# Kernel optimization log

Measured on AMD Instinct MI355X. Metric: run time of the kernel, lower is better.

The kernel has to match this reference:

```python
import jax, jax.numpy as jnp
import numpy as np

N = 65536        # number of encoding vectors (flattened tokens)
K = 1024         # num_embeddings (codebook size)
D = 128          # embedding_dim
BETA = 0.25


def setup_inputs() -> dict:
    key = jax.random.key(0)
    k_enc, k_cb = jax.random.split(key)
    encoding = jax.random.normal(k_enc, (N, D), dtype=jnp.float32)
    # nn.Embedding weight initialized uniform(-1/K, 1/K)
    codebook = jax.random.uniform(k_cb, (K, D), dtype=jnp.float32,
                                  minval=-1.0 / K, maxval=1.0 / K)
    return {"encoding": encoding, "codebook": codebook}


def reference(encoding, codebook):
    # Nearest codebook entry per row. argmin of L2 distance == argmin of
    # squared distance; expand ||e - w||^2 = ||e||^2 - 2 e.w + ||w||^2.
    # ||e||^2 is constant per row, so it does not affect the argmin.
    scores = (-2.0 * jnp.einsum('nd,kd->nk', encoding, codebook)
              + jnp.sum(codebook * codebook, axis=-1)[None, :])  # [N, K]
    quantized_index = jnp.argmin(scores, axis=-1)                # [N] int
    quantized_embedding = codebook[quantized_index]              # [N, D] gather == onehot @ W

    sg = jax.lax.stop_gradient
    commitment_loss = jnp.mean((sg(quantized_embedding) - encoding) ** 2)
    embedding_loss = jnp.mean((quantized_embedding - sg(encoding)) ** 2)
    vq_loss = commitment_loss * BETA + embedding_loss

    # straight-through estimator
    quantized_st = encoding + sg(quantized_embedding - encoding)

    quantized_index = quantized_index[:, None]  # match torch unsqueeze(1) -> [N, 1]
    return (quantized_index, quantized_st, vq_loss, embedding_loss, commitment_loss)
```

## Files before the change

kernel.cpp:

```cpp
#include <hip/hip_runtime.h>


#define NROWS 65536
#define KCB   1024
#define DIM   128
#define DV    32
#define MSE_DENOM 8388608.0f
#define MARGIN 3.0e-5f
#define MARGINS 0.030720f
#define FLAGCAP 16384
#define CSCALE   1024.0f
#define CDESCALE 0.0009765625f

#define WS_CNORM_F  256
#define WS_CN1024_F 1280
#define WS_LIST_B   12288
#define WS_PH_B     77824
#define WS_NEEDED   339968

typedef __attribute__((ext_vector_type(16))) float float16v;
typedef _Float16 half8 __attribute__((ext_vector_type(8)));
union U4H8 { uint4 u; half8 h; };
union F4A  { float4 v; float f[4]; };
union F16V { float16v v; float f[16]; };
union HU   { _Float16 f; unsigned short u; };

__device__ __forceinline__ float fmed3(float a, float b, float c) {
  return __builtin_amdgcn_fmed3f(a, b, c);
}
__device__ __forceinline__ void gload16(const void* g, void* s) {
  __builtin_amdgcn_global_load_lds((const __attribute__((address_space(1))) unsigned int*)g,
                                   (__attribute__((address_space(3))) unsigned int*)s,
                                   16, 0, 0);
}

__global__ __launch_bounds__(64) void vq_prep0(const float* __restrict__ C,
                                               float* __restrict__ wsf) {
  int k = blockIdx.x * 64 + threadIdx.x;
  if (k == 0) { wsf[0] = 0.0f; ((unsigned*)wsf)[1] = 0u; }
  const float4* c4 = (const float4*)C + (size_t)k * DV;
  float s = 0.f;
#pragma unroll 8
  for (int i = 0; i < DV; ++i) {
    float4 v = c4[i];
    s = fmaf(v.x, v.x, s); s = fmaf(v.y, v.y, s);
    s = fmaf(v.z, v.z, s); s = fmaf(v.w, v.w, s);
  }
  wsf[WS_CNORM_F + k]  = s;
  wsf[WS_CN1024_F + k] = s * CSCALE;
}

__global__ __launch_bounds__(256) void vq_pack(const float* __restrict__ C,
                                               uint4* __restrict__ PH) {
  int g = blockIdx.x * 256 + threadIdx.x;
  int mt = g >> 9, s = (g >> 6) & 7, l = g & 63;
  int cw = mt * 32 + (l & 31);
  int k0 = s * 16 + (l >> 5) * 8;
  const float* src = C + (size_t)cw * DIM + k0;
  float4 x0 = *(const float4*)src;
  float4 x1 = *(const float4*)(src + 4);
  unsigned h[8];
  {
    float v[8] = {x0.x, x0.y, x0.z, x0.w, x1.x, x1.y, x1.z, x1.w};
#pragma unroll
    for (int j = 0; j < 8; ++j) { HU u; u.f = (_Float16)(CSCALE * v[j]); h[j] = u.u; }
  }
  PH[g] = make_uint4(h[0] | (h[1] << 16), h[2] | (h[3] << 16),
                     h[4] | (h[5] << 16), h[6] | (h[7] << 16));
}

__global__ __launch_bounds__(256, 4) void vq_main8(const float* __restrict__ E,
                                                   const float* __restrict__ C,
                                                   float* __restrict__ wsf,
                                                   float* __restrict__ out) {
  __shared__ uint4 SH[2][1024];
  __shared__ __align__(16) float CN[1024];
  __shared__ float X1[64], X2[64];
  __shared__ int   XI[64];
  __shared__ int   BI[64];

  const int tid  = threadIdx.x;
  const int w    = tid >> 6;
  const int l    = tid & 63;
  const int half = l >> 5;
  const int rr   = l & 31;
  const int pair = w >> 1;
  const int rw   = w & 1;
  const int row0 = blockIdx.x * 64;
  const int row  = row0 + rw * 32 + rr;

  const uint4* PHg = (const uint4*)((const char*)wsf + WS_PH_B);

  {
    uint4* base = &SH[0][0];
    gload16(PHg + tid,                  base + tid);
    gload16(PHg + 256 + tid,            base + 256 + tid);
    gload16(PHg + 16 * 512 + tid,       base + 512 + tid);
    gload16(PHg + 16 * 512 + 256 + tid, base + 768 + tid);
    gload16(((const uint4*)(wsf + WS_CN1024_F)) + tid, ((uint4*)CN) + tid);
  }

  half8 beh[8];
  float s2 = 0.f;
  const float* erow = E + (size_t)row * DIM + half * 8;
#pragma unroll
  for (int s = 0; s < 8; ++s) {
    float4 x0 = *(const float4*)(erow + s * 16);
    float4 x1 = *(const float4*)(erow + s * 16 + 4);
    float v[8] = {x0.x, x0.y, x0.z, x0.w, x1.x, x1.y, x1.z, x1.w};
#pragma unroll
    for (int j = 0; j < 8; ++j) {
      float y = v[j];
      s2 = fmaf(y, y, s2);
      beh[s][j] = (_Float16)(-2.f * y);
    }
  }

  asm volatile("s_waitcnt vmcnt(0)" ::: "memory");
  __syncthreads();

  float m1 = 3.0e38f, m2 = 3.0e38f;
  int   bi = 0;

  for (int st = 0; st < 16; ++st) {
    const int buf = st & 1;
    const int tg  = pair * 16 + st;
    if (st < 15) {
      uint4* nb = &SH[buf ^ 1][0];
      const uint4* s0 = PHg + (size_t)(st + 1) * 512;
      const uint4* s1 = PHg + (size_t)(17 + st) * 512;
      gload16(s0 + tid,       nb + tid);
      gload16(s0 + 256 + tid, nb + 256 + tid);
      gload16(s1 + tid,       nb + 512 + tid);
      gload16(s1 + 256 + tid, nb + 768 + tid);
    }

    F16V accA, accB;
#pragma unroll
    for (int q = 0; q < 4; ++q) {
      F4A c; c.v = *(const float4*)&CN[tg * 32 + q * 8 + half * 4];
      accA.f[q * 4 + 0] = c.f[0]; accA.f[q * 4 + 1] = c.f[1];
      accA.f[q * 4 + 2] = c.f[2]; accA.f[q * 4 + 3] = c.f[3];
    }
    accB.v = (float16v){0,0,0,0,0,0,0,0,0,0,0,0,0,0,0,0};
#pragma unroll
    for (int s = 0; s < 8; s += 2) {
      U4H8 h0, h1;
      h0.u = SH[buf][pair * 512 + s * 64 + l];
      h1.u = SH[buf][pair * 512 + (s + 1) * 64 + l];
      accA.v = __builtin_amdgcn_mfma_f32_32x32x16_f16(h0.h, beh[s],     accA.v, 0, 0, 0);
      accB.v = __builtin_amdgcn_mfma_f32_32x32x16_f16(h1.h, beh[s + 1], accB.v, 0, 0, 0);
    }

    const int kb = tg * 32 + half * 4;
#pragma unroll
    for (int reg = 0; reg < 16; ++reg) {
      float sc = accA.f[reg] + accB.f[reg];
      bool nb_ = sc < m1;
      m2 = fmed3(sc, m1, m2);
      m1 = fminf(sc, m1);
      bi = nb_ ? (kb + (reg >> 2) * 8 + (reg & 3)) : bi;
    }

    asm volatile("s_waitcnt vmcnt(0)" ::: "memory");
    __syncthreads();
  }

  {
    float om1 = __shfl_xor(m1, 32, 64);
    float om2 = __shfl_xor(m2, 32, 64);
    int   obi = __shfl_xor(bi, 32, 64);
    float nsv = fminf(fminf(m2, om2), fmaxf(m1, om1));
    if (om1 < m1 || (om1 == m1 && obi < bi)) { m1 = om1; bi = obi; }
    m2 = nsv;
  }
  float en = s2 + __shfl_xor(s2, 32, 64);

  if (pair == 1 && half == 0) {
    X1[rw * 32 + rr] = m1; X2[rw * 32 + rr] = m2; XI[rw * 32 + rr] = bi;
  }
  __syncthreads();

  if (pair == 0 && half == 0) {
    const int r = rw * 32 + rr;
    float xb = X1[r], xs = X2[r];
    int   xi = XI[r];
    float sv = fminf(fminf(m2, xs), fmaxf(m1, xb));
    if (xb < m1 || (xb == m1 && xi < bi)) { m1 = xb; bi = xi; }
    out[row] = (float)bi;
    BI[r] = bi;
    if (sv - m1 < MARGINS) {
      unsigned idx = atomicAdd((unsigned*)wsf + 1, 1u);
      if (idx < FLAGCAP) ((int*)((char*)wsf + WS_LIST_B))[idx] = row;
    }
    float term = fmaf(m1, CDESCALE, en);
#pragma unroll
    for (int off = 16; off > 0; off >>= 1) term += __shfl_down(term, off);
    if (rr == 0) atomicAdd(wsf, term);
  }
  __syncthreads();

  const float4* C4   = (const float4*)C;
  float4*       out4 = (float4*)out;
#pragma unroll
  for (int it = 0; it < 8; ++it) {
    int flat = it * 256 + tid;
    int r = flat >> 5, d4 = flat & 31;
    out4[(NROWS / 4) + (size_t)(row0 + r) * DV + d4] = C4[(size_t)BI[r] * DV + d4];
  }
}

__global__ __launch_bounds__(256) void vq_fix(const float* __restrict__ E,
                                              const float* __restrict__ C,
                                              float* __restrict__ wsf,
                                              float* __restrict__ out) {
  __shared__ float4 eL[4][32];
  __shared__ float  RV[4][4];
  __shared__ int    RI[4][4];
  __shared__ int    RESi[4];
  const int tid = threadIdx.x;
  const int wv  = tid >> 6;
  const int ln  = tid & 63;
  const int* list = (const int*)((const char*)wsf + WS_LIST_B);
  int nf = (int)((const unsigned*)wsf)[1];
  if (nf > FLAGCAP) nf = FLAGCAP;
  const float4* E4 = (const float4*)E;
  const float4* C4 = (const float4*)C;
  const float*  cn = wsf + WS_CNORM_F;
  float4* out4 = (float4*)out;

  for (int g = blockIdx.x; g * 4 < nf; g += gridDim.x) {
    const int base = g * 4;
    if (tid < 128) {
      int r = tid >> 5, d4 = tid & 31;
      int R = (base + r < nf) ? list[base + r] : list[base];
      eL[r][d4] = E4[(size_t)R * DV + d4];
    }
    __syncthreads();
    float bv[4] = {3.0e38f, 3.0e38f, 3.0e38f, 3.0e38f};
    int   bi[4] = {0, 0, 0, 0};
#pragma unroll
    for (int j = 0; j < 4; ++j) {
      int k = j * 256 + tid;
      float d0 = 0.f, d1 = 0.f, d2 = 0.f, d3 = 0.f;
#pragma unroll 4
      for (int d4 = 0; d4 < 32; ++d4) {
        float4 c = C4[(size_t)k * DV + d4];
        float4 e0 = eL[0][d4], e1 = eL[1][d4], e2 = eL[2][d4], e3 = eL[3][d4];
        d0 = fmaf(c.x, e0.x, d0); d0 = fmaf(c.y, e0.y, d0);
        d0 = fmaf(c.z, e0.z, d0); d0 = fmaf(c.w, e0.w, d0);
        d1 = fmaf(c.x, e1.x, d1); d1 = fmaf(c.y, e1.y, d1);
        d1 = fmaf(c.z, e1.z, d1); d1 = fmaf(c.w, e1.w, d1);
        d2 = fmaf(c.x, e2.x, d2); d2 = fmaf(c.y, e2.y, d2);
        d2 = fmaf(c.z, e2.z, d2); d2 = fmaf(c.w, e2.w, d2);
        d3 = fmaf(c.x, e3.x, d3); d3 = fmaf(c.y, e3.y, d3);
        d3 = fmaf(c.z, e3.z, d3); d3 = fmaf(c.w, e3.w, d3);
      }
      float cnk = cn[k];
      float s0 = fmaf(-2.f, d0, cnk);
      float s1 = fmaf(-2.f, d1, cnk);
      float s2 = fmaf(-2.f, d2, cnk);
      float s3 = fmaf(-2.f, d3, cnk);
      if (s0 < bv[0] || (s0 == bv[0] && k < bi[0])) { bv[0] = s0; bi[0] = k; }
      if (s1 < bv[1] || (s1 == bv[1] && k < bi[1])) { bv[1] = s1; bi[1] = k; }
      if (s2 < bv[2] || (s2 == bv[2] && k < bi[2])) { bv[2] = s2; bi[2] = k; }
      if (s3 < bv[3] || (s3 == bv[3] && k < bi[3])) { bv[3] = s3; bi[3] = k; }
    }
#pragma unroll
    for (int off = 32; off > 0; off >>= 1) {
#pragma unroll
      for (int r = 0; r < 4; ++r) {
        float wv_ = __shfl_down(bv[r], off);
        int   ji  = __shfl_down(bi[r], off);
        if (wv_ < bv[r] || (wv_ == bv[r] && ji < bi[r])) { bv[r] = wv_; bi[r] = ji; }
      }
    }
    if (ln == 0) {
#pragma unroll
      for (int r = 0; r < 4; ++r) { RV[wv][r] = bv[r]; RI[wv][r] = bi[r]; }
    }
    __syncthreads();
    if (tid < 4) {
      float v = RV[0][tid]; int i = RI[0][tid];
#pragma unroll
      for (int q = 1; q < 4; ++q) {
        float vv = RV[q][tid]; int ii = RI[q][tid];
        if (vv < v || (vv == v && ii < i)) { v = vv; i = ii; }
      }
      RESi[tid] = i;
      if (base + tid < nf) out[list[base + tid]] = (float)i;
    }
    __syncthreads();
    if (tid < 128) {
      int r = tid >> 5, d4 = tid & 31;
      if (base + r < nf) {
        int R = list[base + r];
        out4[(NROWS / 4) + (size_t)R * DV + d4] = C4[(size_t)RESi[r] * DV + d4];
      }
    }
    __syncthreads();
  }
}

__global__ void vq_final(const float* __restrict__ wsf, float* __restrict__ out) {
  if (threadIdx.x == 0 && blockIdx.x == 0) {
    float mse = wsf[0] / MSE_DENOM;
    out[NROWS + NROWS * DIM + 0] = 1.25f * mse;
    out[NROWS + NROWS * DIM + 1] = mse;
    out[NROWS + NROWS * DIM + 2] = mse;
  }
}

__global__ __launch_bounds__(256) void vq_prep_fb(const float* __restrict__ C,
                                                  float* __restrict__ ws) {
  int k = blockIdx.x * 256 + threadIdx.x;
  if (k == 0) ws[0] = 0.0f;
  const float4* c4 = (const float4*)C + (size_t)k * DV;
  float s = 0.f;
#pragma unroll 8
  for (int i = 0; i < DV; ++i) {
    float4 v = c4[i];
    s = fmaf(v.x, v.x, s); s = fmaf(v.y, v.y, s);
    s = fmaf(v.z, v.z, s); s = fmaf(v.w, v.w, s);
  }
  ws[64 + k] = s;
}

__global__ __launch_bounds__(256) void vq_main_fb(const float* __restrict__ E,
                                                  const float* __restrict__ C,
                                                  const float* __restrict__ cnorm,
                                                  float* __restrict__ out,
                                                  float* __restrict__ lossacc) {
  __shared__ float smem[16384];
  float4* EsV = (float4*)smem;
  float4* CsV = (float4*)(smem + 8192);
  const int tid  = threadIdx.x;
  const int row0 = blockIdx.x * 64;
#pragma unroll
  for (int i = 0; i < 8; ++i) {
    int flat = i * 256 + tid;
    int r = flat >> 5, d4 = flat & 31;
    EsV[r * 32 + (d4 ^ (r & 31))] = ((const float4*)E)[(size_t)(row0 + r) * DV + d4];
  }
  const int tx = tid & 15, ty = tid >> 4;
  int rbase[4], rmask[4];
#pragma unroll
  for (int i = 0; i < 4; ++i) { int r = i * 16 + ty; rbase[i] = r * 32; rmask[i] = r & 31; }
  float bestv[4]; int besti[4];
#pragma unroll
  for (int i = 0; i < 4; ++i) { bestv[i] = 3.0e38f; besti[i] = 0; }
  for (int ch = 0; ch < 16; ++ch) {
    const int k0 = ch * 64;
    __syncthreads();
#pragma unroll
    for (int i = 0; i < 8; ++i) {
      int flat = i * 256 + tid;
      int k = flat >> 5, d4 = flat & 31;
      CsV[k * 32 + (d4 ^ (k & 31))] = ((const float4*)C)[(size_t)(k0 + k) * DV + d4];
    }
    __syncthreads();
    float acc[4][4] = {};
#pragma unroll 8
    for (int d4 = 0; d4 < DV; ++d4) {
      float4 a[4], b[4];
#pragma unroll
      for (int i = 0; i < 4; ++i) a[i] = EsV[rbase[i] + (d4 ^ rmask[i])];
#pragma unroll
      for (int j = 0; j < 4; ++j) { int k = j * 16 + tx; b[j] = CsV[k * 32 + (d4 ^ (k & 31))]; }
#pragma unroll
      for (int i = 0; i < 4; ++i)
#pragma unroll
        for (int j = 0; j < 4; ++j) {
          acc[i][j] = fmaf(a[i].x, b[j].x, acc[i][j]);
          acc[i][j] = fmaf(a[i].y, b[j].y, acc[i][j]);
          acc[i][j] = fmaf(a[i].z, b[j].z, acc[i][j]);
          acc[i][j] = fmaf(a[i].w, b[j].w, acc[i][j]);
        }
    }
#pragma unroll
    for (int j = 0; j < 4; ++j) {
      int kg = k0 + j * 16 + tx;
      float cnv = cnorm[kg];
#pragma unroll
      for (int i = 0; i < 4; ++i) {
        float s = fmaf(-2.0f, acc[i][j], cnv);
        if (s < bestv[i] || (s == bestv[i] && kg < besti[i])) { bestv[i] = s; besti[i] = kg; }
      }
    }
  }
  float* Rv = smem + 8192;
  int*   Ri = (int*)(smem + 9216);
  int*   BIf = (int*)(smem + 10240);
  __syncthreads();
#pragma unroll
  for (int i = 0; i < 4; ++i) {
    int r = i * 16 + ty;
    Rv[r * 16 + tx] = bestv[i];
    Ri[r * 16 + tx] = besti[i];
  }
  __syncthreads();
  if (tid < 64) {
    const int r = tid;
    float bv = Rv[r * 16]; int bi = Ri[r * 16];
#pragma unroll
    for (int t = 1; t < 16; ++t) {
      float v = Rv[r * 16 + t]; int ii = Ri[r * 16 + t];
      if (v < bv || (v == bv && ii < bi)) { bv = v; bi = ii; }
    }
    float en = 0.f;
#pragma unroll 8
    for (int d4 = 0; d4 < DV; ++d4) {
      float4 v = EsV[r * 32 + (d4 ^ (r & 31))];
      en = fmaf(v.x, v.x, en); en = fmaf(v.y, v.y, en);
      en = fmaf(v.z, v.z, en); en = fmaf(v.w, v.w, en);
    }
    out[row0 + r] = (float)bi;
    BIf[r] = bi;
    float blocksum = en + bv;
#pragma unroll
    for (int off = 32; off > 0; off >>= 1) blocksum += __shfl_down(blocksum, off);
    if (tid == 0) atomicAdd(lossacc, blocksum);
  }
  __syncthreads();
  const float4* C4   = (const float4*)C;
  float4*       out4 = (float4*)out;
  for (int flat = tid; flat < 64 * DV; flat += 256) {
    int r = flat >> 5, d4 = flat & 31;
    out4[(NROWS / 4) + (size_t)(row0 + r) * DV + d4] = C4[(size_t)BIf[r] * DV + d4];
  }
}

__global__ void vq_final_fb(const float* __restrict__ ws, float* __restrict__ out) {
  if (threadIdx.x == 0 && blockIdx.x == 0) {
    float mse = ws[0] / MSE_DENOM;
    out[NROWS + NROWS * DIM + 0] = 1.25f * mse;
    out[NROWS + NROWS * DIM + 1] = mse;
    out[NROWS + NROWS * DIM + 2] = mse;
  }
}

extern "C" void kernel_launch(void* const* d_in, const int* in_sizes, int n_in,
                              void* d_out, int out_size, void* d_ws, size_t ws_size,
                              hipStream_t stream) {
  const float* E = (const float*)d_in[0];
  const float* C = (const float*)d_in[1];
  float* out = (float*)d_out;
  float* wsf = (float*)d_ws;

  if (ws_size >= (size_t)WS_NEEDED) {
    uint4* PH = (uint4*)((char*)d_ws + WS_PH_B);
    vq_prep0<<<16, 64, 0, stream>>>(C, wsf);
    vq_pack<<<64, 256, 0, stream>>>(C, PH);
    vq_main8<<<NROWS / 64, 256, 0, stream>>>(E, C, wsf, out);
    vq_fix<<<512, 256, 0, stream>>>(E, C, wsf, out);
    vq_final<<<1, 64, 0, stream>>>(wsf, out);
  } else {
    vq_prep_fb<<<4, 256, 0, stream>>>(C, wsf);
    vq_main_fb<<<NROWS / 64, 256, 0, stream>>>(E, C, wsf + 64, out, wsf);
    vq_final_fb<<<1, 64, 0, stream>>>(wsf, out);
  }
}
```

Measured before the change: 161.0 us.

## Triple-buffer codebook tiles in LDS and merge helper kernels to cut launches

The main kernel moves from double to triple buffering of the packed fp16 codebook tiles in LDS. It prefetches two stages ahead and waits with a partial vmcnt plus a single barrier per iteration, instead of a full drain and sync at the end of each step. The two prep kernels are merged into one launch, and the final loss-writing kernel is folded into the start of the fix kernel, removing two launches. In exchange the kernel uses more LDS and its launch bound drops from 4 to 3 blocks per CU. One fma order in the fix kernel is also swapped, which changes rounding slightly.

```diff
diff --git a/kernel.cpp b/kernel.cpp
--- a/kernel.cpp
+++ b/kernel.cpp
@@ -34,46 +34,47 @@
                                    16, 0, 0);
 }
 
-__global__ __launch_bounds__(64) void vq_prep0(const float* __restrict__ C,
-                                               float* __restrict__ wsf) {
-  int k = blockIdx.x * 64 + threadIdx.x;
-  if (k == 0) { wsf[0] = 0.0f; ((unsigned*)wsf)[1] = 0u; }
-  const float4* c4 = (const float4*)C + (size_t)k * DV;
-  float s = 0.f;
+__global__ __launch_bounds__(256) void vq_prep_pack(const float* __restrict__ C,
+                                                    float* __restrict__ wsf,
+                                                    uint4* __restrict__ PH) {
+  const int b = blockIdx.x;
+  if (b < 64) {
+    int g = b * 256 + threadIdx.x;
+    int mt = g >> 9, s = (g >> 6) & 7, l = g & 63;
+    int cw = mt * 32 + (l & 31);
+    int k0 = s * 16 + (l >> 5) * 8;
+    const float* src = C + (size_t)cw * DIM + k0;
+    float4 x0 = *(const float4*)src;
+    float4 x1 = *(const float4*)(src + 4);
+    unsigned h[8];
+    {
+      float v[8] = {x0.x, x0.y, x0.z, x0.w, x1.x, x1.y, x1.z, x1.w};
+#pragma unroll
+      for (int j = 0; j < 8; ++j) { HU u; u.f = (_Float16)(CSCALE * v[j]); h[j] = u.u; }
+    }
+    PH[g] = make_uint4(h[0] | (h[1] << 16), h[2] | (h[3] << 16),
+                       h[4] | (h[5] << 16), h[6] | (h[7] << 16));
+  } else {
+    int k = (b - 64) * 256 + threadIdx.x;
+    if (k == 0) { wsf[0] = 0.0f; ((unsigned*)wsf)[1] = 0u; }
+    const float4* c4 = (const float4*)C + (size_t)k * DV;
+    float s = 0.f;
 #pragma unroll 8
-  for (int i = 0; i < DV; ++i) {
-    float4 v = c4[i];
-    s = fmaf(v.x, v.x, s); s = fmaf(v.y, v.y, s);
-    s = fmaf(v.z, v.z, s); s = fmaf(v.w, v.w, s);
-  }
-  wsf[WS_CNORM_F + k]  = s;
-  wsf[WS_CN1024_F + k] = s * CSCALE;
-}
-
-__global__ __launch_bounds__(256) void vq_pack(const float* __restrict__ C,
-                                               uint4* __restrict__ PH) {
-  int g = blockIdx.x * 256 + threadIdx.x;
-  int mt = g >> 9, s = (g >> 6) & 7, l = g & 63;
-  int cw = mt * 32 + (l & 31);
-  int k0 = s * 16 + (l >> 5) * 8;
-  const float* src = C + (size_t)cw * DIM + k0;
-  float4 x0 = *(const float4*)src;
-  float4 x1 = *(const float4*)(src + 4);
-  unsigned h[8];
-  {
-    float v[8] = {x0.x, x0.y, x0.z, x0.w, x1.x, x1.y, x1.z, x1.w};
-#pragma unroll
-    for (int j = 0; j < 8; ++j) { HU u; u.f = (_Float16)(CSCALE * v[j]); h[j] = u.u; }
-  }
-  PH[g] = make_uint4(h[0] | (h[1] << 16), h[2] | (h[3] << 16),
-                     h[4] | (h[5] << 16), h[6] | (h[7] << 16));
-}
-
-__global__ __launch_bounds__(256, 4) void vq_main8(const float* __restrict__ E,
-                                                   const float* __restrict__ C,
-                                                   float* __restrict__ wsf,
-                                                   float* __restrict__ out) {
-  __shared__ uint4 SH[2][1024];
+    for (int i = 0; i < DV; ++i) {
+      float4 v = c4[i];
+      s = fmaf(v.x, v.x, s); s = fmaf(v.y, v.y, s);
+      s = fmaf(v.z, v.z, s); s = fmaf(v.w, v.w, s);
+    }
+    wsf[WS_CNORM_F + k]  = s;
+    wsf[WS_CN1024_F + k] = s * CSCALE;
+  }
+}
+
+__global__ __launch_bounds__(256, 3) void vq_main10(const float* __restrict__ E,
+                                                    const float* __restrict__ C,
+                                                    float* __restrict__ wsf,
+                                                    float* __restrict__ out) {
+  __shared__ uint4 SH[3][1024];
   __shared__ __align__(16) float CN[1024];
   __shared__ float X1[64], X2[64];
   __shared__ int   XI[64];
@@ -90,15 +91,7 @@
   const int row  = row0 + rw * 32 + rr;
 
   const uint4* PHg = (const uint4*)((const char*)wsf + WS_PH_B);
-
-  {
-    uint4* base = &SH[0][0];
-    gload16(PHg + tid,                  base + tid);
-    gload16(PHg + 256 + tid,            base + 256 + tid);
-    gload16(PHg + 16 * 512 + tid,       base + 512 + tid);
-    gload16(PHg + 16 * 512 + 256 + tid, base + 768 + tid);
-    gload16(((const uint4*)(wsf + WS_CN1024_F)) + tid, ((uint4*)CN) + tid);
-  }
+  const uint4* CNg = (const uint4*)(wsf + WS_CN1024_F);
 
   half8 beh[8];
   float s2 = 0.f;
@@ -115,26 +108,46 @@
       beh[s][j] = (_Float16)(-2.f * y);
     }
   }
-
-  asm volatile("s_waitcnt vmcnt(0)" ::: "memory");
-  __syncthreads();
+  __builtin_amdgcn_sched_barrier(0);
+
+  gload16(CNg + tid, ((uint4*)CN) + tid);
+  {
+    const uint4* s0 = PHg;
+    const uint4* s1 = PHg + 16 * 512;
+    gload16(s0 + tid,       &SH[0][0] + tid);
+    gload16(s0 + 256 + tid, &SH[0][0] + 256 + tid);
+    gload16(s1 + tid,       &SH[0][0] + 512 + tid);
+    gload16(s1 + 256 + tid, &SH[0][0] + 768 + tid);
+    const uint4* t0 = PHg + 512;
+    const uint4* t1 = PHg + 17 * 512;
+    gload16(t0 + tid,       &SH[1][0] + tid);
+    gload16(t0 + 256 + tid, &SH[1][0] + 256 + tid);
+    gload16(t1 + tid,       &SH[1][0] + 512 + tid);
+    gload16(t1 + 256 + tid, &SH[1][0] + 768 + tid);
+  }
+  __builtin_amdgcn_sched_barrier(0);
 
   float m1 = 3.0e38f, m2 = 3.0e38f;
   int   bi = 0;
+  int   cur = 0, nxt = 2;
 
   for (int st = 0; st < 16; ++st) {
-    const int buf = st & 1;
-    const int tg  = pair * 16 + st;
-    if (st < 15) {
-      uint4* nb = &SH[buf ^ 1][0];
-      const uint4* s0 = PHg + (size_t)(st + 1) * 512;
-      const uint4* s1 = PHg + (size_t)(17 + st) * 512;
+    if (st < 15) asm volatile("s_waitcnt vmcnt(4)" ::: "memory");
+    else         asm volatile("s_waitcnt vmcnt(0)" ::: "memory");
+    __builtin_amdgcn_s_barrier();
+    asm volatile("" ::: "memory");
+
+    if (st < 14) {
+      const uint4* s0 = PHg + (size_t)(st + 2) * 512;
+      const uint4* s1 = PHg + (size_t)(18 + st) * 512;
+      uint4* nb = &SH[nxt][0];
       gload16(s0 + tid,       nb + tid);
       gload16(s0 + 256 + tid, nb + 256 + tid);
       gload16(s1 + tid,       nb + 512 + tid);
       gload16(s1 + 256 + tid, nb + 768 + tid);
     }
 
+    const int tg = pair * 16 + st;
     F16V accA, accB;
 #pragma unroll
     for (int q = 0; q < 4; ++q) {
@@ -146,8 +159,8 @@
 #pragma unroll
     for (int s = 0; s < 8; s += 2) {
       U4H8 h0, h1;
-      h0.u = SH[buf][pair * 512 + s * 64 + l];
-      h1.u = SH[buf][pair * 512 + (s + 1) * 64 + l];
+      h0.u = SH[cur][pair * 512 + s * 64 + l];
+      h1.u = SH[cur][pair * 512 + (s + 1) * 64 + l];
       accA.v = __builtin_amdgcn_mfma_f32_32x32x16_f16(h0.h, beh[s],     accA.v, 0, 0, 0);
       accB.v = __builtin_amdgcn_mfma_f32_32x32x16_f16(h1.h, beh[s + 1], accB.v, 0, 0, 0);
     }
@@ -162,8 +175,8 @@
       bi = nb_ ? (kb + (reg >> 2) * 8 + (reg & 3)) : bi;
     }
 
-    asm volatile("s_waitcnt vmcnt(0)" ::: "memory");
-    __syncthreads();
+    cur = (cur == 2) ? 0 : cur + 1;
+    nxt = (nxt == 2) ? 0 : nxt + 1;
   }
 
   {
@@ -221,6 +234,14 @@
   const int tid = threadIdx.x;
   const int wv  = tid >> 6;
   const int ln  = tid & 63;
+
+  if (blockIdx.x == 0 && tid == 0) {
+    float mse = wsf[0] / MSE_DENOM;
+    out[NROWS + NROWS * DIM + 0] = 1.25f * mse;
+    out[NROWS + NROWS * DIM + 1] = mse;
+    out[NROWS + NROWS * DIM + 2] = mse;
+  }
+
   const int* list = (const int*)((const char*)wsf + WS_LIST_B);
   int nf = (int)((const unsigned*)wsf)[1];
   if (nf > FLAGCAP) nf = FLAGCAP;
@@ -254,7 +275,7 @@
         d2 = fmaf(c.x, e2.x, d2); d2 = fmaf(c.y, e2.y, d2);
         d2 = fmaf(c.z, e2.z, d2); d2 = fmaf(c.w, e2.w, d2);
         d3 = fmaf(c.x, e3.x, d3); d3 = fmaf(c.y, e3.y, d3);
-        d3 = fmaf(c.z, e3.z, d3); d3 = fmaf(c.w, e3.w, d3);
+        d3 = fmaf(c.w, e3.w, d3); d3 = fmaf(c.z, e3.z, d3);
       }
       float cnk = cn[k];
       float s0 = fmaf(-2.f, d0, cnk);
@@ -299,15 +320,6 @@
       }
     }
     __syncthreads();
-  }
-}
-
-__global__ void vq_final(const float* __restrict__ wsf, float* __restrict__ out) {
-  if (threadIdx.x == 0 && blockIdx.x == 0) {
-    float mse = wsf[0] / MSE_DENOM;
-    out[NROWS + NROWS * DIM + 0] = 1.25f * mse;
-    out[NROWS + NROWS * DIM + 1] = mse;
-    out[NROWS + NROWS * DIM + 2] = mse;
   }
 }
 
@@ -449,11 +461,9 @@
 
   if (ws_size >= (size_t)WS_NEEDED) {
     uint4* PH = (uint4*)((char*)d_ws + WS_PH_B);
-    vq_prep0<<<16, 64, 0, stream>>>(C, wsf);
-    vq_pack<<<64, 256, 0, stream>>>(C, PH);
-    vq_main8<<<NROWS / 64, 256, 0, stream>>>(E, C, wsf, out);
+    vq_prep_pack<<<68, 256, 0, stream>>>(C, wsf, PH);
+    vq_main10<<<NROWS / 64, 256, 0, stream>>>(E, C, wsf, out);
     vq_fix<<<512, 256, 0, stream>>>(E, C, wsf, out);
-    vq_final<<<1, 64, 0, stream>>>(wsf, out);
   } else {
     vq_prep_fb<<<4, 256, 0, stream>>>(C, wsf);
     vq_main_fb<<<NROWS / 64, 256, 0, stream>>>(E, C, wsf + 64, out, wsf);
```

New measurement: 163.4 us. About the same (+1.5%).
